# Kernel optimization log

Measured on AMD Instinct MI355X. Metric: run time of the kernel, lower is better.

## Reference

```python
import jax, jax.numpy as jnp
import numpy as np

N, D_IN, D_LAT, K = 65536, 1024, 128, 512


def setup_inputs() -> dict:
    key = jax.random.key(0)
    k1, k2, k3 = jax.random.split(key, 3)
    x = jax.random.normal(k1, (N, D_IN), dtype=jnp.float32)
    W = jax.random.normal(k2, (D_IN, D_LAT), dtype=jnp.float32) * 0.02
    b = jnp.zeros((D_LAT,), dtype=jnp.float32)
    centroids = jax.random.normal(k3, (K, D_LAT), dtype=jnp.float32)
    return {"x": x, "W": W, "b": b, "centroids": centroids}


def reference(x, W, b, centroids):
    alpha = 1.0
    # encoder: single linear layer -> latent l [N, D_LAT]
    l = x @ W + b
    # dist_to_centroids: vectorized squared-Euclidean cdist [N, K]
    # ||l - c||^2 = ||l||^2 + ||c||^2 - 2 l.c
    D = (jnp.sum(l * l, axis=1, keepdims=True)
         + jnp.sum(centroids * centroids, axis=1)
         - 2.0 * (l @ centroids.T))
    # Student's t-distribution kernel
    num = jnp.power(1.0 + D / alpha, -(alpha + 1.0) / 2.0)
    Q = num / jnp.sum(num, axis=1, keepdims=True)
    # target distribution
    Fq = jnp.sum(Q, axis=0)            # [K]
    num2 = (Q * Q) / Fq                # [N, K]
    P = num2 / jnp.sum(num2, axis=1, keepdims=True)
    return (l, Q, P)
```

## Files before the change

### kernel.cpp

```cpp
#include <hip/hip_runtime.h>

#define NROWS 65536
#define DIN   1024
#define DLAT  128
#define KC    512

typedef __attribute__((ext_vector_type(8))) short bf16x8;
typedef __attribute__((ext_vector_type(4))) float f32x4;

#define GLDS16(gp, lp)                                                          \
    __builtin_amdgcn_global_load_lds((const __attribute__((address_space(1))) void*)(gp), \
                                     (__attribute__((address_space(3))) void*)(lp), 16, 0, 0)

__device__ inline short f2bf(float f) {
    unsigned u = __float_as_uint(f);
    return (short)((u + 0x7FFFu + ((u >> 16) & 1u)) >> 16);
}

__global__ __launch_bounds__(256) void prep_convert(const float* __restrict__ W,
                                                    const float* __restrict__ C,
                                                    short* __restrict__ Wt,
                                                    short* __restrict__ cb) {
    int idx = blockIdx.x * 256 + threadIdx.x;
    if (idx < DLAT * DIN) {
        int n = idx >> 10, k = idx & 1023;
        Wt[idx] = f2bf(W[k * DLAT + n]);
    } else {
        int i2 = idx - DLAT * DIN;
        if (i2 < KC * DLAT) cb[i2] = f2bf(C[i2]);
    }
}

__global__ __launch_bounds__(64) void prep_csq(const float* __restrict__ C,
                                               float* __restrict__ csq) {
    int row = blockIdx.x;
    int lane = threadIdx.x;
    float a = C[row * DLAT + lane];
    float b = C[row * DLAT + 64 + lane];
    float s = a * a + b * b;
    #pragma unroll
    for (int m = 32; m >= 1; m >>= 1) s += __shfl_xor(s, m, 64);
    if (lane == 0) csq[row] = s;
}

__global__ __launch_bounds__(256) void gemm1(const float* __restrict__ x,
                                             const short* __restrict__ Wt,
                                             const float* __restrict__ bias,
                                             float* __restrict__ lout) {
    __shared__ char lds[65536];
    const int t = threadIdx.x;
    const int wid = t >> 6, lane = t & 63;
    const int l16 = lane & 15, lhi = lane >> 4;
    const int row0 = blockIdx.x * 64;

    const float* xsrc = x + (long)(row0 + (t >> 4)) * DIN + (((t & 15) ^ ((t >> 4) & 15)) << 2);
    const short* wsrc = Wt + (long)(t >> 3) * DIN + (((t & 7) ^ ((t >> 3) & 7)) << 3);
    const int lofs = t * 16;

    f32x4 acc[8];
    #pragma unroll
    for (int i = 0; i < 8; ++i) acc[i] = (f32x4){0.f, 0.f, 0.f, 0.f};

    {
        char* xb = lds;
        char* wb = lds + 16384;
        #pragma unroll
        for (int j = 0; j < 4; ++j) {
            GLDS16(xsrc + j * 16 * DIN, xb + lofs + j * 4096);
            GLDS16(wsrc + j * 32 * DIN, wb + lofs + j * 4096);
        }
    }
    __syncthreads();

    int cur = 0;
    const int arow = wid * 16 + l16;
    for (int kc = 0; kc < 16; ++kc) {
        if (kc < 15) {
            char* xb = lds + (cur ^ 1) * 32768;
            char* wb = xb + 16384;
            const float* xp = xsrc + (kc + 1) * 64;
            const short* wp = wsrc + (kc + 1) * 64;
            #pragma unroll
            for (int j = 0; j < 4; ++j) {
                GLDS16(xp + j * 16 * DIN, xb + lofs + j * 4096);
                GLDS16(wp + j * 32 * DIN, wb + lofs + j * 4096);
            }
        }
        const float* xs = (const float*)(lds + cur * 32768);
        const short* wl = (const short*)(lds + cur * 32768 + 16384);
        #pragma unroll
        for (int ks = 0; ks < 2; ++ks) {
            const int c4 = ks * 8 + lhi * 2;
            const float4 va0 = *(const float4*)(xs + arow * 64 + ((c4 ^ l16) << 2));
            const float4 va1 = *(const float4*)(xs + arow * 64 + (((c4 + 1) ^ l16) << 2));
            bf16x8 af;
            af[0] = f2bf(va0.x); af[1] = f2bf(va0.y); af[2] = f2bf(va0.z); af[3] = f2bf(va0.w);
            af[4] = f2bf(va1.x); af[5] = f2bf(va1.y); af[6] = f2bf(va1.z); af[7] = f2bf(va1.w);
            const int c8 = ks * 4 + lhi;
            #pragma unroll
            for (int nb = 0; nb < 8; ++nb) {
                const int n = nb * 16 + l16;
                const bf16x8 bf = *(const bf16x8*)(wl + n * 64 + ((c8 ^ (n & 7)) << 3));
                acc[nb] = __builtin_amdgcn_mfma_f32_16x16x32_bf16(af, bf, acc[nb], 0, 0, 0);
            }
        }
        __syncthreads();
        cur ^= 1;
    }

    #pragma unroll
    for (int nb = 0; nb < 8; ++nb) {
        int col = nb * 16 + l16;
        float bv = bias[col];
        #pragma unroll
        for (int r = 0; r < 4; ++r) {
            int row = row0 + wid * 16 + lhi * 4 + r;
            lout[(long)row * DLAT + col] = acc[nb][r] + bv;
        }
    }
}

__global__ __launch_bounds__(256, 1) void gemm2_q(const float* __restrict__ lout,
                                                  const short* __restrict__ cb,
                                                  const float* __restrict__ csq,
                                                  float* __restrict__ Qout,
                                                  float* __restrict__ partial) {
    const int wid = threadIdx.x >> 6, lane = threadIdx.x & 63;
    const int l16 = lane & 15, lhi = lane >> 4;
    const int row0 = blockIdx.x * 64 + wid * 16;

    bf16x8 af[4];
    float sq = 0.f;
    const float* lrow = lout + (long)(row0 + l16) * DLAT;
    #pragma unroll
    for (int ks = 0; ks < 4; ++ks) {
        const float4* lp = (const float4*)(lrow + ks * 32 + lhi * 8);
        float4 v0 = lp[0], v1 = lp[1];
        sq += v0.x * v0.x + v0.y * v0.y + v0.z * v0.z + v0.w * v0.w
            + v1.x * v1.x + v1.y * v1.y + v1.z * v1.z + v1.w * v1.w;
        bf16x8 a;
        a[0] = f2bf(v0.x); a[1] = f2bf(v0.y); a[2] = f2bf(v0.z); a[3] = f2bf(v0.w);
        a[4] = f2bf(v1.x); a[5] = f2bf(v1.y); a[6] = f2bf(v1.z); a[7] = f2bf(v1.w);
        af[ks] = a;
    }
    sq += __shfl_xor(sq, 16, 64);
    sq += __shfl_xor(sq, 32, 64);
    float lsqr[4];
    #pragma unroll
    for (int r = 0; r < 4; ++r) lsqr[r] = __shfl(sq, lhi * 4 + r, 64);

    f32x4 numv[32];
    float rsum[4] = {0.f, 0.f, 0.f, 0.f};
    #pragma unroll
    for (int nb = 0; nb < 32; ++nb) {
        f32x4 acc = (f32x4){0.f, 0.f, 0.f, 0.f};
        const short* cbase = cb + (nb * 16 + l16) * DLAT;
        #pragma unroll
        for (int ks = 0; ks < 4; ++ks) {
            const bf16x8 bf = *(const bf16x8*)(cbase + ks * 32 + lhi * 8);
            acc = __builtin_amdgcn_mfma_f32_16x16x32_bf16(af[ks], bf, acc, 0, 0, 0);
        }
        float cs = csq[nb * 16 + l16];
        f32x4 nm;
        #pragma unroll
        for (int r = 0; r < 4; ++r) {
            float Dv = lsqr[r] + cs - 2.f * acc[r];
            float v = 1.f / (1.f + Dv);
            nm[r] = v;
            rsum[r] += v;
        }
        numv[nb] = nm;
    }
    #pragma unroll
    for (int m = 1; m <= 8; m <<= 1) {
        #pragma unroll
        for (int r = 0; r < 4; ++r) rsum[r] += __shfl_xor(rsum[r], m, 64);
    }
    float inv[4];
    #pragma unroll
    for (int r = 0; r < 4; ++r) inv[r] = 1.f / rsum[r];

    __shared__ float lds_fq[4][KC];
    #pragma unroll
    for (int nb = 0; nb < 32; ++nb) {
        float cp = 0.f;
        #pragma unroll
        for (int r = 0; r < 4; ++r) {
            float q = numv[nb][r] * inv[r];
            Qout[(long)(row0 + lhi * 4 + r) * KC + nb * 16 + l16] = q;
            cp += q;
        }
        cp += __shfl_xor(cp, 16, 64);
        cp += __shfl_xor(cp, 32, 64);
        if (lhi == 0) lds_fq[wid][nb * 16 + l16] = cp;
    }
    __syncthreads();
    for (int c = threadIdx.x; c < KC; c += 256) {
        partial[(long)blockIdx.x * KC + c] =
            lds_fq[0][c] + lds_fq[1][c] + lds_fq[2][c] + lds_fq[3][c];
    }
}

__global__ __launch_bounds__(256) void fq_reduce(const float* __restrict__ partial,
                                                 float* __restrict__ fq) {
    int c = blockIdx.x;
    float s = 0.f;
    #pragma unroll
    for (int i = 0; i < 4; ++i) s += partial[(long)(threadIdx.x + i * 256) * KC + c];
    __shared__ float red[256];
    red[threadIdx.x] = s;
    __syncthreads();
    for (int off = 128; off >= 1; off >>= 1) {
        if (threadIdx.x < off) red[threadIdx.x] += red[threadIdx.x + off];
        __syncthreads();
    }
    if (threadIdx.x == 0) fq[c] = red[0];
}

__global__ __launch_bounds__(256) void p_kernel(const float* __restrict__ Q,
                                                const float* __restrict__ fq,
                                                float* __restrict__ P) {
    const int wid = threadIdx.x >> 6, lane = threadIdx.x & 63;
    const int gw = blockIdx.x * 4 + wid;
    const float4 f0 = *(const float4*)(fq + lane * 8);
    const float4 f1 = *(const float4*)(fq + lane * 8 + 4);
    float inv[8] = {1.f / f0.x, 1.f / f0.y, 1.f / f0.z, 1.f / f0.w,
                    1.f / f1.x, 1.f / f1.y, 1.f / f1.z, 1.f / f1.w};
    for (int it = 0; it < 8; ++it) {
        const long row = gw + (long)it * 8192;
        const float4* qp = (const float4*)(Q + row * KC + lane * 8);
        float4 q0 = qp[0], q1 = qp[1];
        float n[8];
        n[0] = q0.x * q0.x * inv[0]; n[1] = q0.y * q0.y * inv[1];
        n[2] = q0.z * q0.z * inv[2]; n[3] = q0.w * q0.w * inv[3];
        n[4] = q1.x * q1.x * inv[4]; n[5] = q1.y * q1.y * inv[5];
        n[6] = q1.z * q1.z * inv[6]; n[7] = q1.w * q1.w * inv[7];
        float rs = n[0] + n[1] + n[2] + n[3] + n[4] + n[5] + n[6] + n[7];
        #pragma unroll
        for (int m = 1; m <= 32; m <<= 1) rs += __shfl_xor(rs, m, 64);
        float ir = 1.f / rs;
        float4 o0 = {n[0] * ir, n[1] * ir, n[2] * ir, n[3] * ir};
        float4 o1 = {n[4] * ir, n[5] * ir, n[6] * ir, n[7] * ir};
        float4* pp = (float4*)(P + row * KC + lane * 8);
        pp[0] = o0; pp[1] = o1;
    }
}

extern "C" void kernel_launch(void* const* d_in, const int* in_sizes, int n_in,
                              void* d_out, int out_size, void* d_ws, size_t ws_size,
                              hipStream_t stream) {
    const float* x  = (const float*)d_in[0];
    const float* W  = (const float*)d_in[1];
    const float* b  = (const float*)d_in[2];
    const float* C  = (const float*)d_in[3];

    float* out  = (float*)d_out;
    float* lout = out;
    float* Qout = out + (long)NROWS * DLAT;
    float* Pout = Qout + (long)NROWS * KC;

    char*  ws      = (char*)d_ws;
    short* Wt      = (short*)ws;
    short* cb      = (short*)(ws + 262144);
    float* csq     = (float*)(ws + 262144 + 131072);
    float* partial = (float*)(ws + 395264);
    float* fq      = (float*)(ws + 395264 + 2097152);

    hipLaunchKernelGGL(prep_convert, dim3(768),  dim3(256), 0, stream, W, C, Wt, cb);
    hipLaunchKernelGGL(prep_csq,     dim3(512),  dim3(64),  0, stream, C, csq);
    hipLaunchKernelGGL(gemm1,        dim3(1024), dim3(256), 0, stream, x, Wt, b, lout);
    hipLaunchKernelGGL(gemm2_q,      dim3(1024), dim3(256), 0, stream, lout, cb, csq, Qout, partial);
    hipLaunchKernelGGL(fq_reduce,    dim3(512),  dim3(256), 0, stream, partial, fq);
    hipLaunchKernelGGL(p_kernel,     dim3(2048), dim3(256), 0, stream, Qout, fq, Pout);
}
```

Before: 242.4 us.

## Fuse encoder GEMM with Q computation and recompute P from latents

The encoder GEMM and the distance/Q kernel are merged into one kernel. The latent tile is staged through swizzled LDS instead of being re-read from global memory. The P pass no longer reads the 128 MB Q matrix; it reloads the small latent tile and recomputes the distance GEMM and kernel values, folding 1/Fq in during fq_reduce. This trades redundant MFMA work and higher register pressure (launch bounds of 2 blocks) for removing a large global read of Q and one kernel launch.

```diff
diff --git a/kernel.cpp b/kernel.cpp
--- a/kernel.cpp
+++ b/kernel.cpp
@@ -43,10 +43,14 @@
     if (lane == 0) csq[row] = s;
 }
 
-__global__ __launch_bounds__(256) void gemm1(const float* __restrict__ x,
-                                             const short* __restrict__ Wt,
-                                             const float* __restrict__ bias,
-                                             float* __restrict__ lout) {
+__global__ __launch_bounds__(256, 2) void fused_aq(const float* __restrict__ x,
+                                                   const short* __restrict__ Wt,
+                                                   const float* __restrict__ bias,
+                                                   const short* __restrict__ cb,
+                                                   const float* __restrict__ csq,
+                                                   float* __restrict__ lout,
+                                                   float* __restrict__ Qout,
+                                                   float* __restrict__ partial) {
     __shared__ char lds[65536];
     const int t = threadIdx.x;
     const int wid = t >> 6, lane = t & 63;
@@ -108,23 +112,117 @@
         cur ^= 1;
     }
 
+    float* l_lds = (float*)lds;
     #pragma unroll
     for (int nb = 0; nb < 8; ++nb) {
-        int col = nb * 16 + l16;
-        float bv = bias[col];
-        #pragma unroll
-        for (int r = 0; r < 4; ++r) {
-            int row = row0 + wid * 16 + lhi * 4 + r;
-            lout[(long)row * DLAT + col] = acc[nb][r] + bv;
-        }
-    }
-}
-
-__global__ __launch_bounds__(256, 1) void gemm2_q(const float* __restrict__ lout,
-                                                  const short* __restrict__ cb,
-                                                  const float* __restrict__ csq,
-                                                  float* __restrict__ Qout,
-                                                  float* __restrict__ partial) {
+        const int col = nb * 16 + l16;
+        const float bv = bias[col];
+        const int slot = col >> 2, e = col & 3;
+        #pragma unroll
+        for (int r = 0; r < 4; ++r) {
+            const int row = wid * 16 + lhi * 4 + r;
+            const float v = acc[nb][r] + bv;
+            lout[(long)(row0 + row) * DLAT + col] = v;
+            l_lds[row * 128 + ((slot ^ (row & 15)) << 2) + e] = v;
+        }
+    }
+    __syncthreads();
+
+    float* lds_fq = (float*)(lds + 32768);
+    const int row0w = row0 + wid * 16;
+
+    bf16x8 af2[4];
+    float sq = 0.f;
+    #pragma unroll
+    for (int ks = 0; ks < 4; ++ks) {
+        const int s0 = 8 * ks + 2 * lhi;
+        const float4 v0 = *(const float4*)(l_lds + arow * 128 + ((s0 ^ l16) << 2));
+        const float4 v1 = *(const float4*)(l_lds + arow * 128 + (((s0 + 1) ^ l16) << 2));
+        sq += v0.x * v0.x + v0.y * v0.y + v0.z * v0.z + v0.w * v0.w
+            + v1.x * v1.x + v1.y * v1.y + v1.z * v1.z + v1.w * v1.w;
+        bf16x8 a;
+        a[0] = f2bf(v0.x); a[1] = f2bf(v0.y); a[2] = f2bf(v0.z); a[3] = f2bf(v0.w);
+        a[4] = f2bf(v1.x); a[5] = f2bf(v1.y); a[6] = f2bf(v1.z); a[7] = f2bf(v1.w);
+        af2[ks] = a;
+    }
+    sq += __shfl_xor(sq, 16, 64);
+    sq += __shfl_xor(sq, 32, 64);
+    float lsqr[4];
+    #pragma unroll
+    for (int r = 0; r < 4; ++r) lsqr[r] = __shfl(sq, lhi * 4 + r, 64);
+
+    f32x4 numv[32];
+    float rsum[4] = {0.f, 0.f, 0.f, 0.f};
+    #pragma unroll
+    for (int nb = 0; nb < 32; ++nb) {
+        f32x4 s2 = (f32x4){0.f, 0.f, 0.f, 0.f};
+        const short* cbase = cb + (nb * 16 + l16) * DLAT;
+        #pragma unroll
+        for (int ks = 0; ks < 4; ++ks) {
+            const bf16x8 bf = *(const bf16x8*)(cbase + ks * 32 + lhi * 8);
+            s2 = __builtin_amdgcn_mfma_f32_16x16x32_bf16(af2[ks], bf, s2, 0, 0, 0);
+        }
+        const float cs = csq[nb * 16 + l16];
+        f32x4 nm;
+        #pragma unroll
+        for (int r = 0; r < 4; ++r) {
+            float Dv = lsqr[r] + cs - 2.f * s2[r];
+            float v = 1.f / (1.f + Dv);
+            nm[r] = v;
+            rsum[r] += v;
+        }
+        numv[nb] = nm;
+    }
+    #pragma unroll
+    for (int m = 1; m <= 8; m <<= 1) {
+        #pragma unroll
+        for (int r = 0; r < 4; ++r) rsum[r] += __shfl_xor(rsum[r], m, 64);
+    }
+    float inv[4];
+    #pragma unroll
+    for (int r = 0; r < 4; ++r) inv[r] = 1.f / rsum[r];
+
+    #pragma unroll
+    for (int nb = 0; nb < 32; ++nb) {
+        float cp = 0.f;
+        #pragma unroll
+        for (int r = 0; r < 4; ++r) {
+            float q = numv[nb][r] * inv[r];
+            Qout[(long)(row0w + lhi * 4 + r) * KC + nb * 16 + l16] = q;
+            cp += q;
+        }
+        cp += __shfl_xor(cp, 16, 64);
+        cp += __shfl_xor(cp, 32, 64);
+        if (lhi == 0) lds_fq[wid * KC + nb * 16 + l16] = cp;
+    }
+    __syncthreads();
+    for (int c = t; c < KC; c += 256) {
+        partial[(long)blockIdx.x * KC + c] =
+            lds_fq[0 * KC + c] + lds_fq[1 * KC + c] + lds_fq[2 * KC + c] + lds_fq[3 * KC + c];
+    }
+}
+
+__global__ __launch_bounds__(256) void fq_reduce(const float* __restrict__ partial,
+                                                 float* __restrict__ fqinv) {
+    int c = blockIdx.x;
+    float s = 0.f;
+    #pragma unroll
+    for (int i = 0; i < 4; ++i) s += partial[(long)(threadIdx.x + i * 256) * KC + c];
+    __shared__ float red[256];
+    red[threadIdx.x] = s;
+    __syncthreads();
+    for (int off = 128; off >= 1; off >>= 1) {
+        if (threadIdx.x < off) red[threadIdx.x] += red[threadIdx.x + off];
+        __syncthreads();
+    }
+    if (threadIdx.x == 0) fqinv[c] = 1.f / red[0];
+}
+
+__global__ __launch_bounds__(256, 2) void p_recompute(const float* __restrict__ lout,
+                                                      const short* __restrict__ cb,
+                                                      const float* __restrict__ csq,
+                                                      const float* __restrict__ fqinv,
+                                                      float* __restrict__ P) {
     const int wid = threadIdx.x >> 6, lane = threadIdx.x & 63;
     const int l16 = lane & 15, lhi = lane >> 4;
     const int row0 = blockIdx.x * 64 + wid * 16;
@@ -149,27 +247,29 @@
     #pragma unroll
     for (int r = 0; r < 4; ++r) lsqr[r] = __shfl(sq, lhi * 4 + r, 64);
 
-    f32x4 numv[32];
+    f32x4 uv[32];
     float rsum[4] = {0.f, 0.f, 0.f, 0.f};
     #pragma unroll
     for (int nb = 0; nb < 32; ++nb) {
-        f32x4 acc = (f32x4){0.f, 0.f, 0.f, 0.f};
+        f32x4 s2 = (f32x4){0.f, 0.f, 0.f, 0.f};
         const short* cbase = cb + (nb * 16 + l16) * DLAT;
         #pragma unroll
         for (int ks = 0; ks < 4; ++ks) {
             const bf16x8 bf = *(const bf16x8*)(cbase + ks * 32 + lhi * 8);
-            acc = __builtin_amdgcn_mfma_f32_16x16x32_bf16(af[ks], bf, acc, 0, 0, 0);
-        }
-        float cs = csq[nb * 16 + l16];
-        f32x4 nm;
-        #pragma unroll
-        for (int r = 0; r < 4; ++r) {
-            float Dv = lsqr[r] + cs - 2.f * acc[r];
-            float v = 1.f / (1.f + Dv);
-            nm[r] = v;
+            s2 = __builtin_amdgcn_mfma_f32_16x16x32_bf16(af[ks], bf, s2, 0, 0, 0);
+        }
+        const float cs = csq[nb * 16 + l16];
+        const float fqi = fqinv[nb * 16 + l16];
+        f32x4 u;
+        #pragma unroll
+        for (int r = 0; r < 4; ++r) {
+            float Dv = lsqr[r] + cs - 2.f * s2[r];
+            float nm = 1.f / (1.f + Dv);
+            float v = nm * nm * fqi;
+            u[r] = v;
             rsum[r] += v;
         }
-        numv[nb] = nm;
+        uv[nb] = u;
     }
     #pragma unroll
     for (int m = 1; m <= 8; m <<= 1) {
@@ -180,69 +280,12 @@
     #pragma unroll
     for (int r = 0; r < 4; ++r) inv[r] = 1.f / rsum[r];
 
-    __shared__ float lds_fq[4][KC];
     #pragma unroll
     for (int nb = 0; nb < 32; ++nb) {
-        float cp = 0.f;
-        #pragma unroll
-        for (int r = 0; r < 4; ++r) {
-            float q = numv[nb][r] * inv[r];
-            Qout[(long)(row0 + lhi * 4 + r) * KC + nb * 16 + l16] = q;
-            cp += q;
-        }
-        cp += __shfl_xor(cp, 16, 64);
-        cp += __shfl_xor(cp, 32, 64);
-        if (lhi == 0) lds_fq[wid][nb * 16 + l16] = cp;
-    }
-    __syncthreads();
-    for (int c = threadIdx.x; c < KC; c += 256) {
-        partial[(long)blockIdx.x * KC + c] =
-            lds_fq[0][c] + lds_fq[1][c] + lds_fq[2][c] + lds_fq[3][c];
-    }
-}
-
-__global__ __launch_bounds__(256) void fq_reduce(const float* __restrict__ partial,
-                                                 float* __restrict__ fq) {
-    int c = blockIdx.x;
-    float s = 0.f;
-    #pragma unroll
-    for (int i = 0; i < 4; ++i) s += partial[(long)(threadIdx.x + i * 256) * KC + c];
-    __shared__ float red[256];
-    red[threadIdx.x] = s;
-    __syncthreads();
-    for (int off = 128; off >= 1; off >>= 1) {
-        if (threadIdx.x < off) red[threadIdx.x] += red[threadIdx.x + off];
-        __syncthreads();
-    }
-    if (threadIdx.x == 0) fq[c] = red[0];
-}
-
-__global__ __launch_bounds__(256) void p_kernel(const float* __restrict__ Q,
-                                                const float* __restrict__ fq,
-                                                float* __restrict__ P) {
-    const int wid = threadIdx.x >> 6, lane = threadIdx.x & 63;
-    const int gw = blockIdx.x * 4 + wid;
-    const float4 f0 = *(const float4*)(fq + lane * 8);
-    const float4 f1 = *(const float4*)(fq + lane * 8 + 4);
-    float inv[8] = {1.f / f0.x, 1.f / f0.y, 1.f / f0.z, 1.f / f0.w,
-                    1.f / f1.x, 1.f / f1.y, 1.f / f1.z, 1.f / f1.w};
-    for (int it = 0; it < 8; ++it) {
-        const long row = gw + (long)it * 8192;
-        const float4* qp = (const float4*)(Q + row * KC + lane * 8);
-        float4 q0 = qp[0], q1 = qp[1];
-        float n[8];
-        n[0] = q0.x * q0.x * inv[0]; n[1] = q0.y * q0.y * inv[1];
-        n[2] = q0.z * q0.z * inv[2]; n[3] = q0.w * q0.w * inv[3];
-        n[4] = q1.x * q1.x * inv[4]; n[5] = q1.y * q1.y * inv[5];
-        n[6] = q1.z * q1.z * inv[6]; n[7] = q1.w * q1.w * inv[7];
-        float rs = n[0] + n[1] + n[2] + n[3] + n[4] + n[5] + n[6] + n[7];
-        #pragma unroll
-        for (int m = 1; m <= 32; m <<= 1) rs += __shfl_xor(rs, m, 64);
-        float ir = 1.f / rs;
-        float4 o0 = {n[0] * ir, n[1] * ir, n[2] * ir, n[3] * ir};
-        float4 o1 = {n[4] * ir, n[5] * ir, n[6] * ir, n[7] * ir};
-        float4* pp = (float4*)(P + row * KC + lane * 8);
-        pp[0] = o0; pp[1] = o1;
+        #pragma unroll
+        for (int r = 0; r < 4; ++r) {
+            P[(long)(row0 + lhi * 4 + r) * KC + nb * 16 + l16] = uv[nb][r] * inv[r];
+        }
     }
 }
 
@@ -264,12 +307,13 @@
     short* cb      = (short*)(ws + 262144);
     float* csq     = (float*)(ws + 262144 + 131072);
     float* partial = (float*)(ws + 395264);
-    float* fq      = (float*)(ws + 395264 + 2097152);
+    float* fqinv   = (float*)(ws + 395264 + 2097152);
 
     hipLaunchKernelGGL(prep_convert, dim3(768),  dim3(256), 0, stream, W, C, Wt, cb);
     hipLaunchKernelGGL(prep_csq,     dim3(512),  dim3(64),  0, stream, C, csq);
-    hipLaunchKernelGGL(gemm1,        dim3(1024), dim3(256), 0, stream, x, Wt, b, lout);
-    hipLaunchKernelGGL(gemm2_q,      dim3(1024), dim3(256), 0, stream, lout, cb, csq, Qout, partial);
-    hipLaunchKernelGGL(fq_reduce,    dim3(512),  dim3(256), 0, stream, partial, fq);
-    hipLaunchKernelGGL(p_kernel,     dim3(2048), dim3(256), 0, stream, Qout, fq, Pout);
-}
+    hipLaunchKernelGGL(fused_aq,     dim3(1024), dim3(256), 0, stream,
+                       x, Wt, b, cb, csq, lout, Qout, partial);
+    hipLaunchKernelGGL(fq_reduce,    dim3(512),  dim3(256), 0, stream, partial, fqinv);
+    hipLaunchKernelGGL(p_recompute,  dim3(1024), dim3(256), 0, stream,
+                       lout, cb, csq, fqinv, Pout);
+}
```

Result: slower. 272.8 us (+12.6%).
